# Optimization experiments

Hardware: AMD Instinct MI355X
Metric: run time of the kernel (lower is better)

Reference implementation:

```python
import jax, jax.numpy as jnp
import numpy as np

NU, NX = 32, 128
NF = 2 * NX  # n_feat
NIN = NU + NX


def setup_inputs() -> dict:
    key = jax.random.key(0)
    ks = jax.random.split(key, 12)
    std = 1e-4
    inp = {
        "input": jax.random.normal(ks[0], (256, 1024, NU), dtype=jnp.float32),
        "x_step": jax.random.normal(ks[1], (1, 1024, NX), dtype=jnp.float32),
        "dt": jnp.float32(0.01),
        # net_dx_linear: Linear(NIN -> NX, no bias)
        "W_lin": std * jax.random.normal(ks[2], (NX, NIN), dtype=jnp.float32),
        # net_dx_nonlinear: Linear(NIN->NF) ReLU Linear(NF->NF) ReLU Linear(NF->NX)
        "W1": std * jax.random.normal(ks[3], (NF, NIN), dtype=jnp.float32),
        "b1": jnp.zeros((NF,), jnp.float32),
        "W2": std * jax.random.normal(ks[4], (NF, NF), dtype=jnp.float32),
        "b2": jnp.zeros((NF,), jnp.float32),
        "W3": std * jax.random.normal(ks[5], (NX, NF), dtype=jnp.float32),
        "b3": jnp.zeros((NX,), jnp.float32),
        # net_output: Linear(NX->NF) ReLU Linear(NF->NF) ReLU Linear(NF->NX)
        "Wo1": std * jax.random.normal(ks[6], (NF, NX), dtype=jnp.float32),
        "bo1": jnp.zeros((NF,), jnp.float32),
        "Wo2": std * jax.random.normal(ks[7], (NF, NF), dtype=jnp.float32),
        "bo2": jnp.zeros((NF,), jnp.float32),
        "Wo3": std * jax.random.normal(ks[8], (NX, NF), dtype=jnp.float32),
        "bo3": jnp.zeros((NX,), jnp.float32),
    }
    return inp


def reference(input, x_step, dt, W_lin, W1, b1, W2, b2, W3, b3,
              Wo1, bo1, Wo2, bo2, Wo3, bo3):
    dt_half = dt / 2.0
    dt_sixth = dt / 6.0

    def dx_net(x, u):
        z = jnp.concatenate((x, u), axis=1)          # [B, NX+NU]
        lin = z @ W_lin.T                             # [B, NX]
        h = jax.nn.relu(z @ W1.T + b1)
        h = jax.nn.relu(h @ W2.T + b2)
        return lin + (h @ W3.T + b3)

    def out_net(x):
        h = jax.nn.relu(x @ Wo1.T + bo1)
        h = jax.nn.relu(h @ Wo2.T + bo2)
        return h @ Wo3.T + bo3

    def step(x, u):
        k1 = dx_net(x, u)
        k2 = dx_net(x + dt_half * k1, u)
        k3 = dx_net(x + dt_half * k2, u)
        k4 = dx_net(x + dt * k3, u)
        x_new = x + dt_sixth * (k1 + 2.0 * k2 + 2.0 * k3 + k4)
        return x_new, out_net(x_new)

    x0 = x_step[0]                                    # [B, NX]
    x_final, y_all = jax.lax.scan(step, x0, input)    # y_all: [nt, B, NX]
    return (y_all, x_final)
```

## Files before the change

kernel.cpp:

```cpp
#include <hip/hip_runtime.h>


#define TSTEPS 256
#define BATCH  1024
#define NUQ    32
#define NXQ    128
#define NFQ    256
#define NINQ   160
#define NY     ((size_t)TSTEPS * BATCH * NXQ)

typedef __attribute__((ext_vector_type(8))) short bf16x8;
typedef __attribute__((ext_vector_type(4))) short s16x4;
typedef __attribute__((ext_vector_type(4))) float f32x4;
typedef __attribute__((ext_vector_type(8))) int i32x8;
typedef __attribute__((ext_vector_type(4))) int i32x4;
typedef unsigned short u16;

__device__ __forceinline__ u16 f2b(float f) {
  unsigned u = __float_as_uint(f);
  u = (u + 0x7FFFu + ((u >> 16) & 1u)) >> 16;
  return (u16)u;
}
__device__ __forceinline__ unsigned cvtpk(float a, float b) {
  unsigned r;
  asm("v_cvt_pk_bf16_f32 %0, %1, %2" : "=v"(r) : "v"(a), "v"(b));
  return r;
}
__device__ __forceinline__ f32x4 mfma16(bf16x8 a, bf16x8 b, f32x4 c) {
  return __builtin_amdgcn_mfma_f32_16x16x32_bf16(a, b, c, 0, 0, 0);
}
__device__ __forceinline__ f32x4 mfmx(i32x8 a, i32x8 b, f32x4 c) {
  return __builtin_amdgcn_mfma_scale_f32_16x16x128_f8f6f4(
      a, b, c, 0, 0, 0, 0x7F7F7F7F, 0, 0x7F7F7F7F);
}
__device__ __forceinline__ bf16x8 ldw8f(const float* p) {
  f32x4 a = *reinterpret_cast<const f32x4*>(p);
  f32x4 b = *reinterpret_cast<const f32x4*>(p + 4);
  bf16x8 r;
  r[0] = (short)f2b(a[0]); r[1] = (short)f2b(a[1]);
  r[2] = (short)f2b(a[2]); r[3] = (short)f2b(a[3]);
  r[4] = (short)f2b(b[0]); r[5] = (short)f2b(b[1]);
  r[6] = (short)f2b(b[2]); r[7] = (short)f2b(b[3]);
  return r;
}
__device__ __forceinline__ i32x8 ldw32f8(const float* p, float s) {
  i32x8 r;
#pragma unroll
  for (int j = 0; j < 8; j++) {
    f32x4 a = *reinterpret_cast<const f32x4*>(p + 4 * j);
    int wd = 0;
    wd = __builtin_amdgcn_cvt_pk_fp8_f32(a[0] * s, a[1] * s, wd, false);
    wd = __builtin_amdgcn_cvt_pk_fp8_f32(a[2] * s, a[3] * s, wd, true);
    r[j] = wd;
  }
  return r;
}
__device__ __forceinline__ void bar_lds() {
  asm volatile("s_waitcnt lgkmcnt(0)" ::: "memory");
  __builtin_amdgcn_s_barrier();
  asm volatile("" ::: "memory");
}

#define ZOFF  0
#define H1OFF 4096
#define H2OFF 8192
#define SMEMB 12288

__global__ __launch_bounds__(512, 2)
void scan_kernel(const float* __restrict__ uin,
                 const float* __restrict__ x0,
                 const float* __restrict__ dtp,
                 const float* __restrict__ Wlin,
                 const float* __restrict__ W1,
                 const float* __restrict__ b1,
                 const float* __restrict__ W2,
                 const float* __restrict__ b2,
                 const float* __restrict__ W3,
                 const float* __restrict__ b3,
                 u16* __restrict__ xall,
                 float* __restrict__ out)
{
  __shared__ __align__(16) char smem[SMEMB];

  const int tid  = threadIdx.x;
  const int wg   = blockIdx.x;
  const int lane = tid & 63;
  const int v    = tid >> 6;
  const int ln   = lane & 15;
  const int q    = lane >> 4;

  const float dt  = dtp[0];
  const float dth = 0.5f * dt;
  const float dt6 = dt * (1.0f / 6.0f);
  const f32x4 zero4 = {0.f, 0.f, 0.f, 0.f};

  const int wby = 256 * (q >> 1) + 16 * ln + 8 * (q & 1);
  const int g4  = ((ln >> 2) & 3) << 4;
  const int o8a = (512 * v + 32 * ln + 4 * q) ^ g4;
  const int o8b = o8a ^ 16;
  const int rbs = (512 * q + 32 * ln) ^ g4;

  bf16x8 wc[5][2];
  bf16x8 wl[5];
  i32x8  w2x[2][2];
  i32x8  w3x[2];
#pragma unroll
  for (int kt = 0; kt < 5; kt++) {
#pragma unroll
    for (int i = 0; i < 2; i++)
      wc[kt][i] = ldw8f(W1 + (size_t)(16 * (2 * v + i) + ln) * NINQ + 32 * kt + 8 * q);
    wl[kt] = ldw8f(Wlin + (size_t)(16 * v + ln) * NINQ + 32 * kt + 8 * q);
  }
#pragma unroll
  for (int b = 0; b < 2; b++) {
#pragma unroll
    for (int i = 0; i < 2; i++)
      w2x[b][i] = ldw32f8(W2 + (size_t)(16 * (2 * v + i) + ln) * NFQ + 128 * b + 32 * q,
                          0x1p11f);
    w3x[b] = ldw32f8(W3 + (size_t)(16 * v + ln) * NFQ + 128 * b + 32 * q, 0x1p11f);
  }

  f32x4 bb1s[2], bb2s[2], bb3;
#pragma unroll
  for (int i = 0; i < 2; i++) {
    f32x4 t1 = *reinterpret_cast<const f32x4*>(b1 + 16 * (2 * v + i) + 4 * q);
    f32x4 t2 = *reinterpret_cast<const f32x4*>(b2 + 16 * (2 * v + i) + 4 * q);
#pragma unroll
    for (int r = 0; r < 4; r++) {
      bb1s[i][r] = t1[r] * 0x1p9f;
      bb2s[i][r] = t2[r] * 0x1p16f;
    }
  }
  bb3 = *reinterpret_cast<const f32x4*>(b3 + 16 * v + 4 * q);

  f32x4 xs, ksum, accl;
  xs = *reinterpret_cast<const f32x4*>(
      x0 + (size_t)(wg * 16 + ln) * NXQ + 16 * v + 4 * q);
  {
    uint2 p;
    p.x = cvtpk(xs[0], xs[1]);
    p.y = cvtpk(xs[2], xs[3]);
    *reinterpret_cast<uint2*>(smem + ZOFF + 512 * v + wby) = p;
  }
  bf16x8 uf = ldw8f(uin + (size_t)(wg * 16 + ln) * NUQ + 8 * q);
  f32x4 ur0 = zero4, ur1 = zero4;
  __syncthreads();

#pragma unroll 1
  for (int t = 0; t < TSTEPS; t++) {
#pragma unroll 1
    for (int e = 0; e < 4; e++) {
      {
        bf16x8 zf[4];
#pragma unroll
        for (int kt = 0; kt < 4; kt++)
          zf[kt] = *reinterpret_cast<const bf16x8*>(smem + ZOFF + 1024 * kt + 16 * lane);
        f32x4 a0 = zero4, a1 = zero4, al = zero4;
#pragma unroll
        for (int kt = 0; kt < 4; kt++) {
          a0 = mfma16(wc[kt][0], zf[kt], a0);
          a1 = mfma16(wc[kt][1], zf[kt], a1);
          al = mfma16(wl[kt], zf[kt], al);
        }
        a0 = mfma16(wc[4][0], uf, a0);
        a1 = mfma16(wc[4][1], uf, a1);
        al = mfma16(wl[4], uf, al);
        accl = al;
#pragma unroll
        for (int i = 0; i < 2; i++) {
          f32x4 d = i ? a1 : a0;
          float e0 = fmaxf(fmaf(d[0], 0x1p9f, bb1s[i][0]), 0.f);
          float e1 = fmaxf(fmaf(d[1], 0x1p9f, bb1s[i][1]), 0.f);
          float e2 = fmaxf(fmaf(d[2], 0x1p9f, bb1s[i][2]), 0.f);
          float e3 = fmaxf(fmaf(d[3], 0x1p9f, bb1s[i][3]), 0.f);
          int wd = 0;
          wd = __builtin_amdgcn_cvt_pk_fp8_f32(e0, e1, wd, false);
          wd = __builtin_amdgcn_cvt_pk_fp8_f32(e2, e3, wd, true);
          *reinterpret_cast<int*>(smem + H1OFF + (i ? o8b : o8a)) = wd;
        }
      }
      bar_lds();
      {
        i32x4 l0 = *reinterpret_cast<const i32x4*>(smem + H1OFF + rbs);
        i32x4 l1 = *reinterpret_cast<const i32x4*>(smem + H1OFF + (rbs ^ 16));
        i32x4 l2 = *reinterpret_cast<const i32x4*>(smem + H1OFF + 2048 + rbs);
        i32x4 l3 = *reinterpret_cast<const i32x4*>(smem + H1OFF + 2048 + (rbs ^ 16));
        i32x8 hb0 = {l0[0], l0[1], l0[2], l0[3], l1[0], l1[1], l1[2], l1[3]};
        i32x8 hb1 = {l2[0], l2[1], l2[2], l2[3], l3[0], l3[1], l3[2], l3[3]};
        f32x4 d0 = mfmx(w2x[0][0], hb0, zero4);
        f32x4 d1 = mfmx(w2x[0][1], hb0, zero4);
        d0 = mfmx(w2x[1][0], hb1, d0);
        d1 = mfmx(w2x[1][1], hb1, d1);
#pragma unroll
        for (int i = 0; i < 2; i++) {
          f32x4 d = i ? d1 : d0;
          float e0 = fmaxf(fmaf(d[0], 0x1p-4f, bb2s[i][0]), 0.f);
          float e1 = fmaxf(fmaf(d[1], 0x1p-4f, bb2s[i][1]), 0.f);
          float e2 = fmaxf(fmaf(d[2], 0x1p-4f, bb2s[i][2]), 0.f);
          float e3 = fmaxf(fmaf(d[3], 0x1p-4f, bb2s[i][3]), 0.f);
          int wd = 0;
          wd = __builtin_amdgcn_cvt_pk_fp8_f32(e0, e1, wd, false);
          wd = __builtin_amdgcn_cvt_pk_fp8_f32(e2, e3, wd, true);
          *reinterpret_cast<int*>(smem + H2OFF + (i ? o8b : o8a)) = wd;
        }
      }
      bar_lds();
      if (e == 0 && t + 1 < TSTEPS) {
        const float* up = uin + ((size_t)(t + 1) * BATCH + wg * 16 + ln) * NUQ + 8 * q;
        ur0 = *reinterpret_cast<const f32x4*>(up);
        ur1 = *reinterpret_cast<const f32x4*>(up + 4);
      }
      if (e == 3 && t + 1 < TSTEPS) {
#pragma unroll
        for (int j = 0; j < 4; j++) {
          uf[j]     = (short)f2b(ur0[j]);
          uf[4 + j] = (short)f2b(ur1[j]);
        }
      }
      {
        i32x4 l0 = *reinterpret_cast<const i32x4*>(smem + H2OFF + rbs);
        i32x4 l1 = *reinterpret_cast<const i32x4*>(smem + H2OFF + (rbs ^ 16));
        i32x4 l2 = *reinterpret_cast<const i32x4*>(smem + H2OFF + 2048 + rbs);
        i32x4 l3 = *reinterpret_cast<const i32x4*>(smem + H2OFF + 2048 + (rbs ^ 16));
        i32x8 gb0 = {l0[0], l0[1], l0[2], l0[3], l1[0], l1[1], l1[2], l1[3]};
        i32x8 gb1 = {l2[0], l2[1], l2[2], l2[3], l3[0], l3[1], l3[2], l3[3]};
        f32x4 ka = mfmx(w3x[0], gb0, zero4);
        ka = mfmx(w3x[1], gb1, ka);
        const float wk = (e == 1 || e == 2) ? 2.0f : 1.0f;
        const float cn = (e == 2) ? dt : dth;
        float xe[4];
#pragma unroll
        for (int r = 0; r < 4; r++) {
          float kv = fmaf(ka[r], 0x1p-27f, accl[r] + bb3[r]);
          if (e == 0) ksum[r] = kv; else ksum[r] += wk * kv;
          if (e == 3) { xs[r] += dt6 * ksum[r]; xe[r] = xs[r]; }
          else        { xe[r] = xs[r] + cn * kv; }
        }
        uint2 p;
        p.x = cvtpk(xe[0], xe[1]);
        p.y = cvtpk(xe[2], xe[3]);
        *reinterpret_cast<uint2*>(smem + ZOFF + 512 * v + wby) = p;
        if (e == 3)
          *reinterpret_cast<uint2*>(
              xall + ((size_t)t * BATCH + wg * 16 + ln) * NXQ + 16 * v + 4 * q) = p;
      }
      bar_lds();
    }
  }

  *reinterpret_cast<f32x4*>(
      out + NY + (size_t)(wg * 16 + ln) * NXQ + 16 * v + 4 * q) = xs;
}

__global__ __launch_bounds__(512, 2)
void outnet_kernel(const u16* __restrict__ xall,
                   const float* __restrict__ Wo1, const float* __restrict__ bo1,
                   const float* __restrict__ Wo2, const float* __restrict__ bo2,
                   const float* __restrict__ Wo3, const float* __restrict__ bo3,
                   float* __restrict__ out,
                   int slab0, int slab_end, int spw)
{
  __shared__ u16 h1[2][16][264];
  __shared__ u16 h2[2][16][264];

  const int tid  = threadIdx.x;
  const int lane = tid & 63;
  const int v    = tid >> 6;
  const int ln   = lane & 15;
  const int q    = lane >> 4;
  const int n1   = 16 * v + ln;
  const int n2   = 128 + n1;
  const f32x4 zero4 = {0.f, 0.f, 0.f, 0.f};

  bf16x8 f1[4][2];
#pragma unroll
  for (int kt = 0; kt < 4; kt++) {
    int k = 32 * kt + 8 * q;
    f1[kt][0] = ldw8f(Wo1 + n1 * NXQ + k);
    f1[kt][1] = ldw8f(Wo1 + n2 * NXQ + k);
  }
  bf16x8 f2[8][2];
#pragma unroll
  for (int kt = 0; kt < 8; kt++) {
    int k = 32 * kt + 8 * q;
    f2[kt][0] = ldw8f(Wo2 + n1 * NFQ + k);
    f2[kt][1] = ldw8f(Wo2 + n2 * NFQ + k);
  }
  bf16x8 f3[8];
#pragma unroll
  for (int kt = 0; kt < 8; kt++)
    f3[kt] = ldw8f(Wo3 + n1 * NFQ + 32 * kt + 8 * q);

  const float c1a = bo1[n1], c1b = bo1[n2];
  const float c2a = bo2[n1], c2b = bo2[n2];
  const float c3  = bo3[n1];

  const int s0  = slab0 + (int)blockIdx.x * spw;
  int cnt = slab_end - s0; if (cnt > spw) cnt = spw;
  if (cnt <= 0) return;

  bf16x8 a[4], an[4];
#pragma unroll
  for (int kt = 0; kt < 4; kt++)
    a[kt] = *reinterpret_cast<const bf16x8*>(
        &xall[((size_t)16 * s0 + ln) * NXQ + 32 * kt + 8 * q]);

#pragma unroll 1
  for (int i = 0; i < cnt; i++) {
    const int s = s0 + i, par = i & 1;
    if (i + 1 < cnt) {
#pragma unroll
      for (int kt = 0; kt < 4; kt++)
        an[kt] = *reinterpret_cast<const bf16x8*>(
            &xall[((size_t)16 * (s + 1) + ln) * NXQ + 32 * kt + 8 * q]);
    }
    {
      f32x4 d0 = zero4, d1 = zero4;
#pragma unroll
      for (int kt = 0; kt < 4; kt++) {
        d0 = mfma16(a[kt], f1[kt][0], d0);
        d1 = mfma16(a[kt], f1[kt][1], d1);
      }
#pragma unroll
      for (int r = 0; r < 4; r++) {
        h1[par][4 * q + r][n1] = f2b(fmaxf(d0[r] + c1a, 0.f));
        h1[par][4 * q + r][n2] = f2b(fmaxf(d1[r] + c1b, 0.f));
      }
    }
    __syncthreads();
    {
      bf16x8 c[8];
#pragma unroll
      for (int kt = 0; kt < 8; kt++)
        c[kt] = *reinterpret_cast<const bf16x8*>(&h1[par][ln][32 * kt + 8 * q]);
      f32x4 e0 = zero4, e1 = zero4;
#pragma unroll
      for (int kt = 0; kt < 8; kt++) {
        e0 = mfma16(c[kt], f2[kt][0], e0);
        e1 = mfma16(c[kt], f2[kt][1], e1);
      }
#pragma unroll
      for (int r = 0; r < 4; r++) {
        h2[par][4 * q + r][n1] = f2b(fmaxf(e0[r] + c2a, 0.f));
        h2[par][4 * q + r][n2] = f2b(fmaxf(e1[r] + c2b, 0.f));
      }
    }
    __syncthreads();
    {
      bf16x8 g[8];
#pragma unroll
      for (int kt = 0; kt < 8; kt++)
        g[kt] = *reinterpret_cast<const bf16x8*>(&h2[par][ln][32 * kt + 8 * q]);
      f32x4 y = zero4;
#pragma unroll
      for (int kt = 0; kt < 8; kt++) y = mfma16(g[kt], f3[kt], y);
#pragma unroll
      for (int r = 0; r < 4; r++)
        out[((size_t)16 * s + 4 * q + r) * NXQ + n1] = y[r] + c3;
    }
#pragma unroll
    for (int kt = 0; kt < 4; kt++) a[kt] = an[kt];
  }
}

extern "C" void kernel_launch(void* const* d_in, const int* in_sizes, int n_in,
                              void* d_out, int out_size, void* d_ws, size_t ws_size,
                              hipStream_t stream) {
  const float* uin  = (const float*)d_in[0];
  const float* x0   = (const float*)d_in[1];
  const float* dtp  = (const float*)d_in[2];
  const float* Wlin = (const float*)d_in[3];
  const float* W1   = (const float*)d_in[4];
  const float* b1   = (const float*)d_in[5];
  const float* W2   = (const float*)d_in[6];
  const float* b2   = (const float*)d_in[7];
  const float* W3   = (const float*)d_in[8];
  const float* b3   = (const float*)d_in[9];
  const float* Wo1  = (const float*)d_in[10];
  const float* bo1  = (const float*)d_in[11];
  const float* Wo2  = (const float*)d_in[12];
  const float* bo2  = (const float*)d_in[13];
  const float* Wo3  = (const float*)d_in[14];
  const float* bo3  = (const float*)d_in[15];
  float* out = (float*)d_out;

  const size_t xall_bytes = NY * sizeof(u16);
  const bool ws_ok = (ws_size >= xall_bytes);
  u16* xall = ws_ok ? (u16*)d_ws : (u16*)d_out;

  scan_kernel<<<dim3(64), dim3(512), 0, stream>>>(
      uin, x0, dtp, Wlin, W1, b1, W2, b2, W3, b3, xall, out);

  const int nslab = TSTEPS * BATCH / 16;
  if (ws_ok) {
    const int spw = 32;
    outnet_kernel<<<dim3(nslab / spw), dim3(512), 0, stream>>>(
        xall, Wo1, bo1, Wo2, bo2, Wo3, bo3, out, 0, nslab, spw);
  } else {
    for (int S = nslab / 2; S >= 1; S >>= 1) {
      int grid = S < 512 ? S : 512;
      int spw  = (S + grid - 1) / grid;
      outnet_kernel<<<dim3(grid), dim3(512), 0, stream>>>(
          xall, Wo1, bo1, Wo2, bo2, Wo3, bo3, out, S, 2 * S, spw);
    }
    outnet_kernel<<<dim3(1), dim3(512), 0, stream>>>(
        xall, Wo1, bo1, Wo2, bo2, Wo3, bo3, out, 0, 1, 1);
  }
}
```

Measured before the change: 1.268 ms.

## Use FP8 MFMA for W1 state layer and the output network

The W1 product on the state part of the scan now uses FP8 scaled MFMA over a new FP8 copy of the state in LDS. The input-dependent contribution (W1 and Wlin times u) is hoisted out of the four RK stages and computed once per time step. The output network is rewritten to match the scan kernel: FP8 weights for layers 2 and 3, transposed MFMA operands, a swizzled FP8 LDS layout and vectorised float4 output stores. This cuts MFMA count and LDS traffic, at the cost of more precision loss from FP8 quantisation of state and hidden activations.

Result: slower. 1.406 ms (+10.9%).

```diff
diff --git a/kernel.cpp b/kernel.cpp
--- a/kernel.cpp
+++ b/kernel.cpp
@@ -10,7 +10,6 @@
 #define NY     ((size_t)TSTEPS * BATCH * NXQ)
 
 typedef __attribute__((ext_vector_type(8))) short bf16x8;
-typedef __attribute__((ext_vector_type(4))) short s16x4;
 typedef __attribute__((ext_vector_type(4))) float f32x4;
 typedef __attribute__((ext_vector_type(8))) int i32x8;
 typedef __attribute__((ext_vector_type(4))) int i32x4;
@@ -55,6 +54,12 @@
   }
   return r;
 }
+__device__ __forceinline__ int pk4f8(float a, float b, float c, float d) {
+  int wd = 0;
+  wd = __builtin_amdgcn_cvt_pk_fp8_f32(a, b, wd, false);
+  wd = __builtin_amdgcn_cvt_pk_fp8_f32(c, d, wd, true);
+  return wd;
+}
 __device__ __forceinline__ void bar_lds() {
   asm volatile("s_waitcnt lgkmcnt(0)" ::: "memory");
   __builtin_amdgcn_s_barrier();
@@ -62,9 +67,10 @@
 }
 
 #define ZOFF  0
-#define H1OFF 4096
-#define H2OFF 8192
-#define SMEMB 12288
+#define Z8OFF 4096
+#define H1OFF 6144
+#define H2OFF 10240
+#define SMEMB 14336
 
 __global__ __launch_bounds__(512, 2)
 void scan_kernel(const float* __restrict__ uin,
@@ -98,19 +104,23 @@
   const int g4  = ((ln >> 2) & 3) << 4;
   const int o8a = (512 * v + 32 * ln + 4 * q) ^ g4;
   const int o8b = o8a ^ 16;
+  const int oz8 = (512 * (v >> 1) + 32 * ln + 16 * (v & 1) + 4 * q) ^ g4;
   const int rbs = (512 * q + 32 * ln) ^ g4;
 
-  bf16x8 wc[5][2];
+  i32x8  w1x8[2];
+  bf16x8 wcu[2];
   bf16x8 wl[5];
   i32x8  w2x[2][2];
   i32x8  w3x[2];
 #pragma unroll
-  for (int kt = 0; kt < 5; kt++) {
-#pragma unroll
-    for (int i = 0; i < 2; i++)
-      wc[kt][i] = ldw8f(W1 + (size_t)(16 * (2 * v + i) + ln) * NINQ + 32 * kt + 8 * q);
+  for (int i = 0; i < 2; i++) {
+    w1x8[i] = ldw32f8(W1 + (size_t)(16 * (2 * v + i) + ln) * NINQ + 32 * q, 0x1p11f);
+    wcu[i]  = ldw8f(W1 + (size_t)(16 * (2 * v + i) + ln) * NINQ + 128 + 8 * q);
+  }
+#pragma unroll
+  for (int kt = 0; kt < 4; kt++)
     wl[kt] = ldw8f(Wlin + (size_t)(16 * v + ln) * NINQ + 32 * kt + 8 * q);
-  }
+  wl[4] = ldw8f(Wlin + (size_t)(16 * v + ln) * NINQ + 128 + 8 * q);
 #pragma unroll
   for (int b = 0; b < 2; b++) {
 #pragma unroll
@@ -141,6 +151,8 @@
     p.x = cvtpk(xs[0], xs[1]);
     p.y = cvtpk(xs[2], xs[3]);
     *reinterpret_cast<uint2*>(smem + ZOFF + 512 * v + wby) = p;
+    *reinterpret_cast<int*>(smem + Z8OFF + oz8) =
+        pk4f8(xs[0], xs[1], xs[2], xs[3]);
   }
   bf16x8 uf = ldw8f(uin + (size_t)(wg * 16 + ln) * NUQ + 8 * q);
   f32x4 ur0 = zero4, ur1 = zero4;
@@ -148,6 +160,12 @@
 
 #pragma unroll 1
   for (int t = 0; t < TSTEPS; t++) {
+    f32x4 uc0 = mfma16(wcu[0], uf, zero4);
+    f32x4 uc1 = mfma16(wcu[1], uf, zero4);
+    f32x4 ucl = mfma16(wl[4], uf, zero4);
+    f32x4 uc0s, uc1s;
+#pragma unroll
+    for (int r = 0; r < 4; r++) { uc0s[r] = uc0[r] * 0x1p11f; uc1s[r] = uc1[r] * 0x1p11f; }
 #pragma unroll 1
     for (int e = 0; e < 4; e++) {
       {
@@ -155,28 +173,27 @@
 #pragma unroll
         for (int kt = 0; kt < 4; kt++)
           zf[kt] = *reinterpret_cast<const bf16x8*>(smem + ZOFF + 1024 * kt + 16 * lane);
-        f32x4 a0 = zero4, a1 = zero4, al = zero4;
-#pragma unroll
-        for (int kt = 0; kt < 4; kt++) {
-          a0 = mfma16(wc[kt][0], zf[kt], a0);
-          a1 = mfma16(wc[kt][1], zf[kt], a1);
-          al = mfma16(wl[kt], zf[kt], al);
-        }
-        a0 = mfma16(wc[4][0], uf, a0);
-        a1 = mfma16(wc[4][1], uf, a1);
-        al = mfma16(wl[4], uf, al);
-        accl = al;
+        i32x4 za = *reinterpret_cast<const i32x4*>(smem + Z8OFF + rbs);
+        i32x4 zb = *reinterpret_cast<const i32x4*>(smem + Z8OFF + (rbs ^ 16));
+        i32x8 zfull = {za[0], za[1], za[2], za[3], zb[0], zb[1], zb[2], zb[3]};
+        f32x4 a0 = mfmx(w1x8[0], zfull, uc0s);
+        f32x4 a1 = mfmx(w1x8[1], zfull, uc1s);
+        f32x4 ala = ucl, alb = zero4;
+        ala = mfma16(wl[0], zf[0], ala);
+        alb = mfma16(wl[1], zf[1], alb);
+        ala = mfma16(wl[2], zf[2], ala);
+        alb = mfma16(wl[3], zf[3], alb);
+#pragma unroll
+        for (int r = 0; r < 4; r++) accl[r] = ala[r] + alb[r];
 #pragma unroll
         for (int i = 0; i < 2; i++) {
           f32x4 d = i ? a1 : a0;
-          float e0 = fmaxf(fmaf(d[0], 0x1p9f, bb1s[i][0]), 0.f);
-          float e1 = fmaxf(fmaf(d[1], 0x1p9f, bb1s[i][1]), 0.f);
-          float e2 = fmaxf(fmaf(d[2], 0x1p9f, bb1s[i][2]), 0.f);
-          float e3 = fmaxf(fmaf(d[3], 0x1p9f, bb1s[i][3]), 0.f);
-          int wd = 0;
-          wd = __builtin_amdgcn_cvt_pk_fp8_f32(e0, e1, wd, false);
-          wd = __builtin_amdgcn_cvt_pk_fp8_f32(e2, e3, wd, true);
-          *reinterpret_cast<int*>(smem + H1OFF + (i ? o8b : o8a)) = wd;
+          float e0 = fmaxf(fmaf(d[0], 0x1p-2f, bb1s[i][0]), 0.f);
+          float e1 = fmaxf(fmaf(d[1], 0x1p-2f, bb1s[i][1]), 0.f);
+          float e2 = fmaxf(fmaf(d[2], 0x1p-2f, bb1s[i][2]), 0.f);
+          float e3 = fmaxf(fmaf(d[3], 0x1p-2f, bb1s[i][3]), 0.f);
+          *reinterpret_cast<int*>(smem + H1OFF + (i ? o8b : o8a)) =
+              pk4f8(e0, e1, e2, e3);
         }
       }
       bar_lds();
@@ -198,10 +215,8 @@
           float e1 = fmaxf(fmaf(d[1], 0x1p-4f, bb2s[i][1]), 0.f);
           float e2 = fmaxf(fmaf(d[2], 0x1p-4f, bb2s[i][2]), 0.f);
           float e3 = fmaxf(fmaf(d[3], 0x1p-4f, bb2s[i][3]), 0.f);
-          int wd = 0;
-          wd = __builtin_amdgcn_cvt_pk_fp8_f32(e0, e1, wd, false);
-          wd = __builtin_amdgcn_cvt_pk_fp8_f32(e2, e3, wd, true);
-          *reinterpret_cast<int*>(smem + H2OFF + (i ? o8b : o8a)) = wd;
+          *reinterpret_cast<int*>(smem + H2OFF + (i ? o8b : o8a)) =
+              pk4f8(e0, e1, e2, e3);
         }
       }
       bar_lds();
@@ -240,6 +255,8 @@
         p.x = cvtpk(xe[0], xe[1]);
         p.y = cvtpk(xe[2], xe[3]);
         *reinterpret_cast<uint2*>(smem + ZOFF + 512 * v + wby) = p;
+        *reinterpret_cast<int*>(smem + Z8OFF + oz8) =
+            pk4f8(xe[0], xe[1], xe[2], xe[3]);
         if (e == 3)
           *reinterpret_cast<uint2*>(
               xall + ((size_t)t * BATCH + wg * 16 + ln) * NXQ + 16 * v + 4 * q) = p;
@@ -260,40 +277,50 @@
                    float* __restrict__ out,
                    int slab0, int slab_end, int spw)
 {
-  __shared__ u16 h1[2][16][264];
-  __shared__ u16 h2[2][16][264];
+  __shared__ __align__(16) char smem[16384];
 
   const int tid  = threadIdx.x;
   const int lane = tid & 63;
   const int v    = tid >> 6;
   const int ln   = lane & 15;
   const int q    = lane >> 4;
-  const int n1   = 16 * v + ln;
-  const int n2   = 128 + n1;
   const f32x4 zero4 = {0.f, 0.f, 0.f, 0.f};
 
+  const int g4  = ((ln >> 2) & 3) << 4;
+  const int o8a = (512 * v + 32 * ln + 4 * q) ^ g4;
+  const int o8b = o8a ^ 16;
+  const int rbs = (512 * q + 32 * ln) ^ g4;
+
   bf16x8 f1[4][2];
 #pragma unroll
-  for (int kt = 0; kt < 4; kt++) {
-    int k = 32 * kt + 8 * q;
-    f1[kt][0] = ldw8f(Wo1 + n1 * NXQ + k);
-    f1[kt][1] = ldw8f(Wo1 + n2 * NXQ + k);
-  }
-  bf16x8 f2[8][2];
-#pragma unroll
-  for (int kt = 0; kt < 8; kt++) {
-    int k = 32 * kt + 8 * q;
-    f2[kt][0] = ldw8f(Wo2 + n1 * NFQ + k);
-    f2[kt][1] = ldw8f(Wo2 + n2 * NFQ + k);
-  }
-  bf16x8 f3[8];
-#pragma unroll
-  for (int kt = 0; kt < 8; kt++)
-    f3[kt] = ldw8f(Wo3 + n1 * NFQ + 32 * kt + 8 * q);
-
-  const float c1a = bo1[n1], c1b = bo1[n2];
-  const float c2a = bo2[n1], c2b = bo2[n2];
-  const float c3  = bo3[n1];
+  for (int kt = 0; kt < 4; kt++)
+#pragma unroll
+    for (int i = 0; i < 2; i++)
+      f1[kt][i] = ldw8f(Wo1 + (size_t)(16 * (2 * v + i) + ln) * NXQ + 32 * kt + 8 * q);
+  i32x8 wo2[2][2];
+#pragma unroll
+  for (int b = 0; b < 2; b++)
+#pragma unroll
+    for (int i = 0; i < 2; i++)
+      wo2[b][i] = ldw32f8(Wo2 + (size_t)(16 * (2 * v + i) + ln) * NFQ + 128 * b + 32 * q,
+                          0x1p11f);
+  i32x8 wo3[2];
+#pragma unroll
+  for (int b = 0; b < 2; b++)
+    wo3[b] = ldw32f8(Wo3 + (size_t)(16 * v + ln) * NFQ + 128 * b + 32 * q, 0x1p11f);
+
+  f32x4 c1s[2], c2s[2], c3;
+#pragma unroll
+  for (int i = 0; i < 2; i++) {
+    f32x4 t1 = *reinterpret_cast<const f32x4*>(bo1 + 16 * (2 * v + i) + 4 * q);
+    f32x4 t2 = *reinterpret_cast<const f32x4*>(bo2 + 16 * (2 * v + i) + 4 * q);
+#pragma unroll
+    for (int r = 0; r < 4; r++) {
+      c1s[i][r] = t1[r] * 0x1p9f;
+      c2s[i][r] = t2[r] * 0x1p16f;
+    }
+  }
+  c3 = *reinterpret_cast<const f32x4*>(bo3 + 16 * v + 4 * q);
 
   const int s0  = slab0 + (int)blockIdx.x * spw;
   int cnt = slab_end - s0; if (cnt > spw) cnt = spw;
@@ -308,6 +335,7 @@
 #pragma unroll 1
   for (int i = 0; i < cnt; i++) {
     const int s = s0 + i, par = i & 1;
+    const int h1o = par * 4096, h2o = 8192 + par * 4096;
     if (i + 1 < cnt) {
 #pragma unroll
       for (int kt = 0; kt < 4; kt++)
@@ -318,45 +346,58 @@
       f32x4 d0 = zero4, d1 = zero4;
 #pragma unroll
       for (int kt = 0; kt < 4; kt++) {
-        d0 = mfma16(a[kt], f1[kt][0], d0);
-        d1 = mfma16(a[kt], f1[kt][1], d1);
-      }
-#pragma unroll
-      for (int r = 0; r < 4; r++) {
-        h1[par][4 * q + r][n1] = f2b(fmaxf(d0[r] + c1a, 0.f));
-        h1[par][4 * q + r][n2] = f2b(fmaxf(d1[r] + c1b, 0.f));
-      }
-    }
-    __syncthreads();
+        d0 = mfma16(f1[kt][0], a[kt], d0);
+        d1 = mfma16(f1[kt][1], a[kt], d1);
+      }
+#pragma unroll
+      for (int i2 = 0; i2 < 2; i2++) {
+        f32x4 d = i2 ? d1 : d0;
+        float e0 = fmaxf(fmaf(d[0], 0x1p9f, c1s[i2][0]), 0.f);
+        float e1 = fmaxf(fmaf(d[1], 0x1p9f, c1s[i2][1]), 0.f);
+        float e2 = fmaxf(fmaf(d[2], 0x1p9f, c1s[i2][2]), 0.f);
+        float e3 = fmaxf(fmaf(d[3], 0x1p9f, c1s[i2][3]), 0.f);
+        *reinterpret_cast<int*>(smem + h1o + (i2 ? o8b : o8a)) =
+            pk4f8(e0, e1, e2, e3);
+      }
+    }
+    bar_lds();
     {
-      bf16x8 c[8];
-#pragma unroll
-      for (int kt = 0; kt < 8; kt++)
-        c[kt] = *reinterpret_cast<const bf16x8*>(&h1[par][ln][32 * kt + 8 * q]);
-      f32x4 e0 = zero4, e1 = zero4;
-#pragma unroll
-      for (int kt = 0; kt < 8; kt++) {
-        e0 = mfma16(c[kt], f2[kt][0], e0);
-        e1 = mfma16(c[kt], f2[kt][1], e1);
-      }
-#pragma unroll
-      for (int r = 0; r < 4; r++) {
-        h2[par][4 * q + r][n1] = f2b(fmaxf(e0[r] + c2a, 0.f));
-        h2[par][4 * q + r][n2] = f2b(fmaxf(e1[r] + c2b, 0.f));
-      }
-    }
-    __syncthreads();
+      i32x4 l0 = *reinterpret_cast<const i32x4*>(smem + h1o + rbs);
+      i32x4 l1 = *reinterpret_cast<const i32x4*>(smem + h1o + (rbs ^ 16));
+      i32x4 l2 = *reinterpret_cast<const i32x4*>(smem + h1o + 2048 + rbs);
+      i32x4 l3 = *reinterpret_cast<const i32x4*>(smem + h1o + 2048 + (rbs ^ 16));
+      i32x8 hb0 = {l0[0], l0[1], l0[2], l0[3], l1[0], l1[1], l1[2], l1[3]};
+      i32x8 hb1 = {l2[0], l2[1], l2[2], l2[3], l3[0], l3[1], l3[2], l3[3]};
+      f32x4 e0v = mfmx(wo2[0][0], hb0, zero4);
+      f32x4 e1v = mfmx(wo2[0][1], hb0, zero4);
+      e0v = mfmx(wo2[1][0], hb1, e0v);
+      e1v = mfmx(wo2[1][1], hb1, e1v);
+#pragma unroll
+      for (int i2 = 0; i2 < 2; i2++) {
+        f32x4 d = i2 ? e1v : e0v;
+        float e0 = fmaxf(fmaf(d[0], 0x1p-4f, c2s[i2][0]), 0.f);
+        float e1 = fmaxf(fmaf(d[1], 0x1p-4f, c2s[i2][1]), 0.f);
+        float e2 = fmaxf(fmaf(d[2], 0x1p-4f, c2s[i2][2]), 0.f);
+        float e3 = fmaxf(fmaf(d[3], 0x1p-4f, c2s[i2][3]), 0.f);
+        *reinterpret_cast<int*>(smem + h2o + (i2 ? o8b : o8a)) =
+            pk4f8(e0, e1, e2, e3);
+      }
+    }
+    bar_lds();
     {
-      bf16x8 g[8];
-#pragma unroll
-      for (int kt = 0; kt < 8; kt++)
-        g[kt] = *reinterpret_cast<const bf16x8*>(&h2[par][ln][32 * kt + 8 * q]);
-      f32x4 y = zero4;
-#pragma unroll
-      for (int kt = 0; kt < 8; kt++) y = mfma16(g[kt], f3[kt], y);
-#pragma unroll
-      for (int r = 0; r < 4; r++)
-        out[((size_t)16 * s + 4 * q + r) * NXQ + n1] = y[r] + c3;
+      i32x4 l0 = *reinterpret_cast<const i32x4*>(smem + h2o + rbs);
+      i32x4 l1 = *reinterpret_cast<const i32x4*>(smem + h2o + (rbs ^ 16));
+      i32x4 l2 = *reinterpret_cast<const i32x4*>(smem + h2o + 2048 + rbs);
+      i32x4 l3 = *reinterpret_cast<const i32x4*>(smem + h2o + 2048 + (rbs ^ 16));
+      i32x8 gb0 = {l0[0], l0[1], l0[2], l0[3], l1[0], l1[1], l1[2], l1[3]};
+      i32x8 gb1 = {l2[0], l2[1], l2[2], l2[3], l3[0], l3[1], l3[2], l3[3]};
+      f32x4 y = mfmx(wo3[0], gb0, zero4);
+      y = mfmx(wo3[1], gb1, y);
+      f32x4 yo;
+#pragma unroll
+      for (int r = 0; r < 4; r++) yo[r] = fmaf(y[r], 0x1p-27f, c3[r]);
+      *reinterpret_cast<f32x4*>(
+          out + ((size_t)16 * s + ln) * NXQ + 16 * v + 4 * q) = yo;
     }
 #pragma unroll
     for (int kt = 0; kt < 4; kt++) a[kt] = an[kt];
```
